# Performance work log

Measured on AMD Instinct MI355X. Metric: run time of the kernel, lower is better.

The kernel has to match this reference:

```python
import jax, jax.numpy as jnp
from jax import lax
import numpy as np

NLAYERS = 3
NHID = 256
NINP = 128
K = 2          # nstride (conv kernel size)
B = 32
W = 512


def _lstm_conv_layer(x_list, hid, ctx, conv_ws, conv_bs, rw, rb, aw):
    """One LSTM_conv(nl=len(conv_ws)) forward.
    x_list: list of [B, H, W]; hid: [nl+1, B, H, K]; ctx: [nl, B, H, K].
    Returns hx_all [B,H,W], cx_all [B,H,W], attn [B,W-1].
    """
    nl = len(conv_ws)
    ig = None
    for j in range(nl):
        # left-pad with last K-1 hidden columns, 'VALID' conv of kernel K -> length W
        padded = jnp.concatenate([hid[j][:, :, 1:], x_list[j]], axis=2)  # [B,H,W+K-1]
        y = lax.conv_general_dilated(padded, conv_ws[j], (1,), 'VALID',
                                     dimension_numbers=('NCH', 'OIH', 'NCH'))
        y = y + conv_bs[j][None, :, None]
        ig = y if ig is None else ig + y          # [B, 4H, W]

    hx0 = hid[nl][:, :, K - 1]                    # [B, H]
    cx0 = ctx[nl - 1][:, :, K - 1]                # [B, H]
    wsz = ig.shape[-1]
    ig_t = jnp.transpose(ig, (2, 0, 1))           # [W, B, 4H]
    not_last = jnp.arange(wsz) < (wsz - 1)

    def step(carry, inp):
        hx, cx = carry
        g_t, nl_flag = inp
        gates = g_t + hx @ rw.T + rb              # [B, 4H]
        i_g, f_g, c_g, o_g = jnp.split(gates, 4, axis=-1)  # torch fused LSTM order
        cx = jax.nn.sigmoid(f_g) * cx + jax.nn.sigmoid(i_g) * jnp.tanh(c_g)
        hx = jax.nn.sigmoid(o_g) * jnp.tanh(cx)
        a = jax.nn.sigmoid(hx @ aw)               # [B]
        hx = jnp.where(nl_flag, hx * a[:, None], hx)  # gate applied except at last step
        return (hx, cx), (hx, cx, a)

    _, (hs, cs, a_s) = lax.scan(step, (hx0, cx0), (ig_t, not_last))
    hx_all = jnp.transpose(hs, (1, 2, 0))         # [B, H, W]
    cx_all = jnp.transpose(cs, (1, 2, 0))
    attn = a_s[:-1].T                             # [B, W-1]
    return hx_all, cx_all, attn


def setup_inputs() -> dict:
    key = jax.random.key(0)
    ks = jax.random.split(key, 10)
    s = 0.02
    return {
        'input':   jax.random.normal(ks[0], (B, NINP, W), jnp.float32),
        'hidden':  jax.random.normal(ks[1], (NLAYERS + 1, B, NHID, K), jnp.float32),
        'context': jax.random.normal(ks[2], (NLAYERS, B, NHID, K), jnp.float32),
        'emb_w':   jax.random.normal(ks[3], (NHID, NINP), jnp.float32) * s,
        'emb_b':   jax.random.normal(ks[4], (NHID,), jnp.float32) * s,
        'conv_w':  jax.random.normal(ks[5], (6, 4 * NHID, NHID, K), jnp.float32) * s,
        'conv_b':  jax.random.normal(ks[6], (6, 4 * NHID), jnp.float32) * s,
        'rec_w':   jax.random.normal(ks[7], (NLAYERS, 4 * NHID, NHID), jnp.float32) * s,
        'rec_b':   jax.random.normal(ks[8], (NLAYERS, 4 * NHID), jnp.float32) * s,
        'attn_w':  jax.random.normal(ks[9], (NLAYERS, NHID), jnp.float32) * s,
    }


def reference(input, hidden, context, emb_w, emb_b, conv_w, conv_b, rec_w, rec_b, attn_w):
    # emb: Conv1d(ninp, nhid, 1)
    x0 = jnp.einsum('oc,bcw->bow', emb_w, input) + emb_b[None, :, None]  # [B,H,W]
    x_list = [x0]
    next_ctx = []
    attns = []
    off = 0
    for l in range(NLAYERS):
        nl = l + 1
        hx_all, cx_all, attn = _lstm_conv_layer(
            x_list, hidden[:nl + 1], context[:nl],
            [conv_w[off + j] for j in range(nl)],
            [conv_b[off + j] for j in range(nl)],
            rec_w[l], rec_b[l], attn_w[l])
        off += nl
        x_list.append(hx_all)
        next_ctx.append(cx_all)
        attns.append(attn)
    x = jnp.stack(x_list, 0)                      # [NLAYERS+1, B, H, W]
    nc = jnp.stack(next_ctx, 0)                   # [NLAYERS, B, H, W]
    attns = jnp.stack(attns, 0)                   # [NLAYERS, B, W-1]
    return x[:, :, :, -K:], nc[:, :, :, -K:], attns
```

## Files before the change

### kernel.cpp

```cpp
#include <hip/hip_runtime.h>


typedef _Float16 h2 __attribute__((ext_vector_type(2)));

static __device__ __forceinline__ float fdot2(unsigned a, unsigned b, float c) {
#if __has_builtin(__builtin_amdgcn_fdot2)
  return __builtin_amdgcn_fdot2(__builtin_bit_cast(h2, a),
                                __builtin_bit_cast(h2, b), c, false);
#else
  h2 x = __builtin_bit_cast(h2, a), y = __builtin_bit_cast(h2, b);
  return c + (float)x[0] * (float)y[0] + (float)x[1] * (float)y[1];
#endif
}

static __device__ __forceinline__ unsigned short f16b(float v) {
  _Float16 h = (_Float16)v;
  return __builtin_bit_cast(unsigned short, h);
}

static __device__ __forceinline__ float sigm(float x) {
  return 1.0f / (1.0f + __expf(-x));
}
static __device__ __forceinline__ float tanh_(float x) {
  return 1.0f - 2.0f / (1.0f + __expf(2.0f * x));
}

__global__ __launch_bounds__(256) void prep_rw(const float* __restrict__ rw,
                                               unsigned* __restrict__ rwp) {
  int idx = blockIdx.x * 256 + threadIdx.x;
  if (idx >= 3 * 131072) return;
  int l = idx / 131072, pos = idx % 131072;
  int tid, rl, j;
  if (pos < 98304) {
    int d = pos >> 9;
    tid = pos & 511;
    rl = d / 24;
    j = d % 24;
  } else {
    int p = pos - 98304;
    int c = p >> 11, rem = p & 2047;
    tid = rem >> 2;
    int k = rem & 3;
    rl = c >> 1;
    j = 24 + (c & 1) * 4 + k;
  }
  int s = tid & 3, u = tid >> 2;
  int row = (rl >> 1) * 256 + (rl & 1) * 128 + u;
  int cp = s * 32 + j;
  const float* src = rw + (l * 1024 + row) * 256 + 2 * cp;
  rwp[idx] = (unsigned)f16b(src[0]) | ((unsigned)f16b(src[1]) << 16);
}

__global__ __launch_bounds__(256) void prep_cw(const float* __restrict__ cw,
                                               unsigned* __restrict__ cwp) {
  int idx = blockIdx.x * 256 + threadIdx.x;
  if (idx >= 6 * 1024 * 2 * 128) return;
  int d = idx & 127, k = (idx >> 7) & 1, o = (idx >> 8) & 1023, jj = idx >> 18;
  const float* src = cw + ((jj * 1024 + o) * 256 + 2 * d) * 2 + k;
  unsigned v = (unsigned)f16b(src[0]) | ((unsigned)f16b(src[2]) << 16);
  cwp[idx] = v;
}

__global__ __launch_bounds__(256) void emb_kernel(
    const float* __restrict__ inp, const float* __restrict__ ew,
    const float* __restrict__ eb, unsigned short* __restrict__ x0f,
    float* __restrict__ out) {
  __shared__ float xt[32][65];
  __shared__ float wt[64][33];
  int b = blockIdx.z, w0 = blockIdx.x * 64, h0 = blockIdx.y * 64;
  int tid = threadIdx.x, tx = tid & 15, ty = tid >> 4;
  float acc[4][4] = {};
  for (int c0 = 0; c0 < 128; c0 += 32) {
    __syncthreads();
#pragma unroll
    for (int i = 0; i < 8; i++) {
      int f = i * 256 + tid, c = f >> 6, wl = f & 63;
      xt[c][wl] = inp[(b * 128 + c0 + c) * 512 + w0 + wl];
    }
#pragma unroll
    for (int i = 0; i < 8; i++) {
      int f = i * 256 + tid, h = f >> 5, c = f & 31;
      wt[h][c] = ew[(h0 + h) * 128 + c0 + c];
    }
    __syncthreads();
#pragma unroll
    for (int c = 0; c < 32; c++) {
      float xv[4], wv[4];
#pragma unroll
      for (int q = 0; q < 4; q++) xv[q] = xt[c][ty * 4 + q];
#pragma unroll
      for (int p = 0; p < 4; p++) wv[p] = wt[tx * 4 + p][c];
#pragma unroll
      for (int q = 0; q < 4; q++)
#pragma unroll
        for (int p = 0; p < 4; p++) acc[q][p] += xv[q] * wv[p];
    }
  }
#pragma unroll
  for (int q = 0; q < 4; q++) {
    int w = w0 + ty * 4 + q;
#pragma unroll
    for (int p = 0; p < 4; p++) {
      int h = h0 + tx * 4 + p;
      float v = acc[q][p] + eb[h];
      x0f[(b * 512 + w) * 256 + h] = f16b(v);
      if (w >= 510) out[(b * 256 + h) * 2 + (w - 510)] = v;
    }
  }
}

__global__ __launch_bounds__(256) void conv_kernel(
    const unsigned short* __restrict__ xf, const unsigned* __restrict__ cwp,
    const float* __restrict__ cb, const float* __restrict__ hidden,
    unsigned short* __restrict__ igf, int l, int off) {
  __shared__ __align__(16) unsigned xs[65][20];
  __shared__ __align__(16) unsigned wsm[2][16][66];
  int b = blockIdx.z, w0 = blockIdx.x * 64, o0 = blockIdx.y * 64;
  int tid = threadIdx.x, tx = tid & 15, ty = tid >> 4;
  float acc[4][4] = {};
  int nl = l + 1;
  for (int j = 0; j < nl; j++) {
    const unsigned* xj = (const unsigned*)(xf + j * 4194304 + b * 512 * 256);
    const unsigned* cwj = cwp + (off + j) * 262144;
    for (int c0 = 0; c0 < 256; c0 += 32) {
      int d0 = c0 >> 1;
      __syncthreads();
#pragma unroll
      for (int i = 0; i < 5; i++) {
        int f = i * 256 + tid;
        if (f < 1040) {
          int col = f >> 4, dw = f & 15;
          int w = w0 - 1 + col;
          unsigned v;
          if (w >= 0) {
            v = xj[w * 128 + d0 + dw];
          } else {
            const float* hp = hidden + ((j * 32 + b) * 256 + 2 * (d0 + dw)) * 2 + 1;
            v = (unsigned)f16b(hp[0]) | ((unsigned)f16b(hp[2]) << 16);
          }
          xs[col][dw] = v;
        }
      }
#pragma unroll
      for (int i = 0; i < 8; i++) {
        int f = i * 256 + tid;
        int oo = f >> 5, k = (f >> 4) & 1, dw = f & 15;
        wsm[k][dw][oo] = cwj[(o0 + oo) * 256 + k * 128 + d0 + dw];
      }
      __syncthreads();
#pragma unroll
      for (int g = 0; g < 4; g++) {
        uint4 xv[5];
#pragma unroll
        for (int q = 0; q < 5; q++)
          xv[q] = *(const uint4*)&xs[ty * 4 + q][g * 4];
#pragma unroll
        for (int p = 0; p < 4; p++) {
          unsigned wv0[4], wv1[4];
#pragma unroll
          for (int r = 0; r < 4; r++) {
            wv0[r] = wsm[0][g * 4 + r][tx * 4 + p];
            wv1[r] = wsm[1][g * 4 + r][tx * 4 + p];
          }
#pragma unroll
          for (int q = 0; q < 4; q++) {
            float a = acc[q][p];
            a = fdot2(wv0[0], xv[q].x, a);
            a = fdot2(wv0[1], xv[q].y, a);
            a = fdot2(wv0[2], xv[q].z, a);
            a = fdot2(wv0[3], xv[q].w, a);
            a = fdot2(wv1[0], xv[q + 1].x, a);
            a = fdot2(wv1[1], xv[q + 1].y, a);
            a = fdot2(wv1[2], xv[q + 1].z, a);
            a = fdot2(wv1[3], xv[q + 1].w, a);
            acc[q][p] = a;
          }
        }
      }
    }
  }
#pragma unroll
  for (int p = 0; p < 4; p++) {
    int o = o0 + tx * 4 + p;
    float bias = 0.f;
    for (int j = 0; j < nl; j++) bias += cb[(off + j) * 1024 + o];
#pragma unroll
    for (int q = 0; q < 4; q++) {
      int w = w0 + ty * 4 + q;
      igf[(b * 512 + w) * 1024 + o] = f16b(acc[q][p] + bias);
    }
  }
}

__global__ __launch_bounds__(512)
__attribute__((amdgpu_waves_per_eu(2, 2)))
void rec_kernel(const _Float16* __restrict__ igf, const unsigned* __restrict__ rwp_l,
                const float* __restrict__ rb, const float* __restrict__ aw,
                const float* __restrict__ hidden, const float* __restrict__ context,
                int l, unsigned short* __restrict__ xnext, float* __restrict__ out) {
  __shared__ __align__(16) uint4 w_lds4[16 * 512];
  __shared__ __align__(16) unsigned short hx_buf[2][256];
  __shared__ float red[2][8];
  int b = blockIdx.x, tid = threadIdx.x;
  int s = tid & 3, u = tid >> 2, lane = tid & 63, wid = tid >> 6;
  int hh = s & 1;
  int u2 = u + 128 * hh;

  unsigned wv[192];
#pragma unroll
  for (int d = 0; d < 192; d++) wv[d] = rwp_l[d * 512 + tid];
#pragma unroll
  for (int d = 0; d < 192; d++) asm volatile("" : "+v"(wv[d]));

  {
    const uint4* g16 = (const uint4*)(rwp_l + 98304);
#pragma unroll
    for (int c = 0; c < 16; c++) w_lds4[c * 512 + tid] = g16[c * 512 + tid];
  }

  float rb0 = rb[u2], rb1 = rb[256 + u2], rb2 = rb[512 + u2], rb3 = rb[768 + u2];
  float awj = aw[u2];
  float cx = context[((l * 32 + b) * 256 + u2) * 2 + 1];
  if (tid < 256)
    hx_buf[1][tid] = f16b(hidden[(((l + 1) * 32 + b) * 256 + tid) * 2 + 1]);
  float h_prev = 0.f;
  __syncthreads();

  const _Float16* igb = igf + (b * 512) * 1024 + u2;

  for (int t = 0; t < 512; t++) {
    int cur = t & 1, prv = cur ^ 1;
    const _Float16* ip = igb + t * 1024;
    float ig0 = (float)ip[0], ig1 = (float)ip[256];
    float ig2 = (float)ip[512], ig3 = (float)ip[768];
    float m_ = 1.0f;
    if (t) {
      const float* rp = red[prv];
      m_ = sigm(((rp[0] + rp[1]) + (rp[2] + rp[3])) +
                ((rp[4] + rp[5]) + (rp[6] + rp[7])));
    }

    float acc[8] = {};
    const uint4* hq = ((const uint4*)hx_buf[prv]) + 8 * s;
#pragma unroll
    for (int q = 0; q < 6; q++) {
      uint4 h = hq[q];
#pragma unroll
      for (int rl = 0; rl < 8; rl++) {
        acc[rl] = fdot2(wv[rl * 24 + q * 4 + 0], h.x, acc[rl]);
        acc[rl] = fdot2(wv[rl * 24 + q * 4 + 1], h.y, acc[rl]);
        acc[rl] = fdot2(wv[rl * 24 + q * 4 + 2], h.z, acc[rl]);
        acc[rl] = fdot2(wv[rl * 24 + q * 4 + 3], h.w, acc[rl]);
      }
    }
#pragma unroll
    for (int q = 6; q < 8; q++) {
      uint4 h = hq[q];
#pragma unroll
      for (int rl = 0; rl < 8; rl++) {
        uint4 lw = w_lds4[(rl * 2 + (q - 6)) * 512 + tid];
        acc[rl] = fdot2(lw.x, h.x, acc[rl]);
        acc[rl] = fdot2(lw.y, h.y, acc[rl]);
        acc[rl] = fdot2(lw.z, h.z, acc[rl]);
        acc[rl] = fdot2(lw.w, h.w, acc[rl]);
      }
    }
#pragma unroll
    for (int rl = 0; rl < 8; rl++) acc[rl] += __shfl_xor(acc[rl], 1);
#pragma unroll
    for (int rl = 0; rl < 8; rl++) acc[rl] += __shfl_xor(acc[rl], 2);

    float di = hh ? acc[1] : acc[0];
    float df = hh ? acc[3] : acc[2];
    float dc = hh ? acc[5] : acc[4];
    float do_ = hh ? acc[7] : acc[6];
    float g_i = ig0 + rb0 + m_ * di;
    float g_f = ig1 + rb1 + m_ * df;
    float g_c = ig2 + rb2 + m_ * dc;
    float g_o = ig3 + rb3 + m_ * do_;
    cx = sigm(g_f) * cx + sigm(g_i) * tanh_(g_c);
    float h_raw = sigm(g_o) * tanh_(cx);

    float part = (s < 2) ? h_raw * awj : 0.f;
#pragma unroll
    for (int sh = 32; sh > 0; sh >>= 1) part += __shfl_xor(part, sh);
    if (lane == 0) red[cur][wid] = part;

    if (s < 2) {
      hx_buf[cur][u2] = f16b(h_raw);
      if (t) {
        float hg = h_prev * m_;
        xnext[(b * 512 + (t - 1)) * 256 + u2] = f16b(hg);
        if (t == 511)
          out[(((l + 1) * 32 + b) * 256 + u2) * 2 + 0] = hg;
      }
      if (t >= 510)
        out[65536 + ((l * 32 + b) * 256 + u2) * 2 + (t - 510)] = cx;
    }
    if (tid == 0 && t) out[114688 + (l * 32 + b) * 511 + (t - 1)] = m_;
    h_prev = h_raw;
    __syncthreads();
  }
  if (s < 2) {
    xnext[(b * 512 + 511) * 256 + u2] = f16b(h_prev);
    out[(((l + 1) * 32 + b) * 256 + u2) * 2 + 1] = h_prev;
  }
}

extern "C" void kernel_launch(void* const* d_in, const int* in_sizes, int n_in,
                              void* d_out, int out_size, void* d_ws,
                              size_t ws_size, hipStream_t stream) {
  const float* input  = (const float*)d_in[0];
  const float* hidden = (const float*)d_in[1];
  const float* context= (const float*)d_in[2];
  const float* emb_w  = (const float*)d_in[3];
  const float* emb_b  = (const float*)d_in[4];
  const float* conv_w = (const float*)d_in[5];
  const float* conv_b = (const float*)d_in[6];
  const float* rec_w  = (const float*)d_in[7];
  const float* rec_b  = (const float*)d_in[8];
  const float* attn_w = (const float*)d_in[9];
  float* out = (float*)d_out;

  char* ws = (char*)d_ws;
  unsigned short* xf16 = (unsigned short*)ws;
  _Float16* igf = (_Float16*)(ws + 33554432);
  unsigned* rwp = (unsigned*)(ws + 67108864);
  unsigned* cwp = (unsigned*)(ws + 68681728);

  hipLaunchKernelGGL(prep_rw, dim3(1536), dim3(256), 0, stream, rec_w, rwp);
  hipLaunchKernelGGL(prep_cw, dim3(6144), dim3(256), 0, stream, conv_w, cwp);
  hipLaunchKernelGGL(emb_kernel, dim3(8, 4, 32), dim3(256), 0, stream,
                     input, emb_w, emb_b, xf16, out);
  int off = 0;
  for (int l = 0; l < 3; l++) {
    hipLaunchKernelGGL(conv_kernel, dim3(8, 16, 32), dim3(256), 0, stream,
                       xf16, cwp, conv_b, hidden, (unsigned short*)igf, l, off);
    hipLaunchKernelGGL(rec_kernel, dim3(32), dim3(512), 0, stream,
                       igf, rwp + l * 131072, rec_b + l * 1024,
                       attn_w + l * 256, hidden, context, l,
                       xf16 + (l + 1) * 4194304, out);
    off += l + 1;
  }
}
```

Measured before the change: 4.405 ms.

## Store recurrent weights in AGPRs, stream a slice from global, use DPP reductions

Recurrent weights are moved from arch VGPRs into accumulation registers (AGPRs) via inline v_accvgpr writes and reads. One column slice of the weights is now streamed from global memory each step instead of being kept in registers. The h-vector read offsets are rotated per lane group to avoid LDS bank conflicts, and the shuffle-based reductions are replaced by DPP row operations. Global output stores are moved to the start of the next step so they leave the critical path. This relieves VGPR pressure at the cost of extra AGPR read instructions and per-step global loads.

New measurement: 6.175 ms. 40.2% more time.

```diff
diff --git a/kernel.cpp b/kernel.cpp
--- a/kernel.cpp
+++ b/kernel.cpp
@@ -13,6 +13,19 @@
 #endif
 }
 
+static __device__ __forceinline__ unsigned aread(unsigned a) {
+  unsigned v;
+  asm volatile("v_accvgpr_read_b32 %0, %1" : "=v"(v) : "a"(a));
+  return v;
+}
+
+template <int CTRL>
+static __device__ __forceinline__ float dpp_add(float x) {
+  int t = __builtin_amdgcn_update_dpp(0, __builtin_bit_cast(int, x), CTRL, 0xf,
+                                      0xf, true);
+  return x + __builtin_bit_cast(float, t);
+}
+
 static __device__ __forceinline__ unsigned short f16b(float v) {
   _Float16 h = (_Float16)v;
   return __builtin_bit_cast(unsigned short, h);
@@ -30,23 +43,39 @@
   int idx = blockIdx.x * 256 + threadIdx.x;
   if (idx >= 3 * 131072) return;
   int l = idx / 131072, pos = idx % 131072;
-  int tid, rl, j;
-  if (pos < 98304) {
+  int tid, rl, i, k;
+  if (pos < 90112) {
     int d = pos >> 9;
     tid = pos & 511;
-    rl = d / 24;
-    j = d % 24;
+    if (d < 160) {
+      rl = d / 20;
+      int rem = d % 20;
+      i = rem >> 2;
+      k = rem & 3;
+    } else {
+      rl = 4 + ((d - 160) >> 2);
+      i = 5;
+      k = (d - 160) & 3;
+    }
+  } else if (pos < 98304) {
+    int p = pos - 90112;
+    rl = p >> 11;
+    int rem = p & 2047;
+    tid = rem >> 2;
+    k = rem & 3;
+    i = 5;
   } else {
     int p = pos - 98304;
     int c = p >> 11, rem = p & 2047;
     tid = rem >> 2;
-    int k = rem & 3;
+    k = rem & 3;
     rl = c >> 1;
-    j = 24 + (c & 1) * 4 + k;
+    i = 6 + (c & 1);
   }
   int s = tid & 3, u = tid >> 2;
   int row = (rl >> 1) * 256 + (rl & 1) * 128 + u;
-  int cp = s * 32 + j;
+  int qeff = (i + 2 * s) & 7;
+  int cp = s * 32 + qeff * 4 + k;
   const float* src = rw + (l * 1024 + row) * 256 + 2 * cp;
   rwp[idx] = (unsigned)f16b(src[0]) | ((unsigned)f16b(src[1]) << 16);
 }
@@ -206,17 +235,23 @@
   int hh = s & 1;
   int u2 = u + 128 * hh;
 
-  unsigned wv[192];
-#pragma unroll
-  for (int d = 0; d < 192; d++) wv[d] = rwp_l[d * 512 + tid];
-#pragma unroll
-  for (int d = 0; d < 192; d++) asm volatile("" : "+v"(wv[d]));
+  unsigned wa[176];
+#pragma unroll
+  for (int d = 0; d < 176; d++) {
+    unsigned v = rwp_l[d * 512 + tid];
+    asm volatile("v_accvgpr_write_b32 %0, %1" : "=a"(wa[d]) : "v"(v));
+  }
 
   {
     const uint4* g16 = (const uint4*)(rwp_l + 98304);
 #pragma unroll
     for (int c = 0; c < 16; c++) w_lds4[c * 512 + tid] = g16[c * 512 + tid];
   }
+  const uint4* gq = ((const uint4*)rwp_l) + 22528;
+
+  int qoff[8];
+#pragma unroll
+  for (int i = 0; i < 8; i++) qoff[i] = (8 * s + ((i + 2 * s) & 7)) * 16;
 
   float rb0 = rb[u2], rb1 = rb[256 + u2], rb2 = rb[512 + u2], rb3 = rb[768 + u2];
   float awj = aw[u2];
@@ -230,35 +265,72 @@
 
   for (int t = 0; t < 512; t++) {
     int cur = t & 1, prv = cur ^ 1;
-    const _Float16* ip = igb + t * 1024;
-    float ig0 = (float)ip[0], ig1 = (float)ip[256];
-    float ig2 = (float)ip[512], ig3 = (float)ip[768];
     float m_ = 1.0f;
     if (t) {
       const float* rp = red[prv];
       m_ = sigm(((rp[0] + rp[1]) + (rp[2] + rp[3])) +
                 ((rp[4] + rp[5]) + (rp[6] + rp[7])));
-    }
+      if (s < 2) {
+        float hg = h_prev * m_;
+        xnext[(b * 512 + (t - 1)) * 256 + u2] = f16b(hg);
+        if (t == 511) {
+          out[(((l + 1) * 32 + b) * 256 + u2) * 2 + 0] = hg;
+          out[65536 + ((l * 32 + b) * 256 + u2) * 2 + 0] = cx;
+        }
+      }
+      if (tid == 0) out[114688 + (l * 32 + b) * 511 + (t - 1)] = m_;
+    }
+    const _Float16* ip = igb + t * 1024;
+    float ig0 = (float)ip[0], ig1 = (float)ip[256];
+    float ig2 = (float)ip[512], ig3 = (float)ip[768];
+    uint4 gw0 = gq[tid], gw1 = gq[512 + tid], gw2 = gq[1024 + tid],
+          gw3 = gq[1536 + tid];
 
     float acc[8] = {};
-    const uint4* hq = ((const uint4*)hx_buf[prv]) + 8 * s;
-#pragma unroll
-    for (int q = 0; q < 6; q++) {
-      uint4 h = hq[q];
+    const char* hb = (const char*)hx_buf[prv];
+#pragma unroll
+    for (int i = 0; i < 5; i++) {
+      uint4 h = *(const uint4*)(hb + qoff[i]);
 #pragma unroll
       for (int rl = 0; rl < 8; rl++) {
-        acc[rl] = fdot2(wv[rl * 24 + q * 4 + 0], h.x, acc[rl]);
-        acc[rl] = fdot2(wv[rl * 24 + q * 4 + 1], h.y, acc[rl]);
-        acc[rl] = fdot2(wv[rl * 24 + q * 4 + 2], h.z, acc[rl]);
-        acc[rl] = fdot2(wv[rl * 24 + q * 4 + 3], h.w, acc[rl]);
-      }
-    }
-#pragma unroll
-    for (int q = 6; q < 8; q++) {
-      uint4 h = hq[q];
+        acc[rl] = fdot2(aread(wa[rl * 20 + i * 4 + 0]), h.x, acc[rl]);
+        acc[rl] = fdot2(aread(wa[rl * 20 + i * 4 + 1]), h.y, acc[rl]);
+        acc[rl] = fdot2(aread(wa[rl * 20 + i * 4 + 2]), h.z, acc[rl]);
+        acc[rl] = fdot2(aread(wa[rl * 20 + i * 4 + 3]), h.w, acc[rl]);
+      }
+    }
+    {
+      uint4 h = *(const uint4*)(hb + qoff[5]);
+      acc[0] = fdot2(gw0.x, h.x, acc[0]);
+      acc[0] = fdot2(gw0.y, h.y, acc[0]);
+      acc[0] = fdot2(gw0.z, h.z, acc[0]);
+      acc[0] = fdot2(gw0.w, h.w, acc[0]);
+      acc[1] = fdot2(gw1.x, h.x, acc[1]);
+      acc[1] = fdot2(gw1.y, h.y, acc[1]);
+      acc[1] = fdot2(gw1.z, h.z, acc[1]);
+      acc[1] = fdot2(gw1.w, h.w, acc[1]);
+      acc[2] = fdot2(gw2.x, h.x, acc[2]);
+      acc[2] = fdot2(gw2.y, h.y, acc[2]);
+      acc[2] = fdot2(gw2.z, h.z, acc[2]);
+      acc[2] = fdot2(gw2.w, h.w, acc[2]);
+      acc[3] = fdot2(gw3.x, h.x, acc[3]);
+      acc[3] = fdot2(gw3.y, h.y, acc[3]);
+      acc[3] = fdot2(gw3.z, h.z, acc[3]);
+      acc[3] = fdot2(gw3.w, h.w, acc[3]);
+#pragma unroll
+      for (int rl = 4; rl < 8; rl++) {
+        acc[rl] = fdot2(aread(wa[160 + (rl - 4) * 4 + 0]), h.x, acc[rl]);
+        acc[rl] = fdot2(aread(wa[160 + (rl - 4) * 4 + 1]), h.y, acc[rl]);
+        acc[rl] = fdot2(aread(wa[160 + (rl - 4) * 4 + 2]), h.z, acc[rl]);
+        acc[rl] = fdot2(aread(wa[160 + (rl - 4) * 4 + 3]), h.w, acc[rl]);
+      }
+    }
+#pragma unroll
+    for (int i = 6; i < 8; i++) {
+      uint4 h = *(const uint4*)(hb + qoff[i]);
 #pragma unroll
       for (int rl = 0; rl < 8; rl++) {
-        uint4 lw = w_lds4[(rl * 2 + (q - 6)) * 512 + tid];
+        uint4 lw = w_lds4[(rl * 2 + (i - 6)) * 512 + tid];
         acc[rl] = fdot2(lw.x, h.x, acc[rl]);
         acc[rl] = fdot2(lw.y, h.y, acc[rl]);
         acc[rl] = fdot2(lw.z, h.z, acc[rl]);
@@ -266,9 +338,9 @@
       }
     }
 #pragma unroll
-    for (int rl = 0; rl < 8; rl++) acc[rl] += __shfl_xor(acc[rl], 1);
-#pragma unroll
-    for (int rl = 0; rl < 8; rl++) acc[rl] += __shfl_xor(acc[rl], 2);
+    for (int rl = 0; rl < 8; rl++) acc[rl] = dpp_add<0xB1>(acc[rl]);
+#pragma unroll
+    for (int rl = 0; rl < 8; rl++) acc[rl] = dpp_add<0x4E>(acc[rl]);
 
     float di = hh ? acc[1] : acc[0];
     float df = hh ? acc[3] : acc[2];
@@ -281,29 +353,24 @@
     cx = sigm(g_f) * cx + sigm(g_i) * tanh_(g_c);
     float h_raw = sigm(g_o) * tanh_(cx);
 
+    if (s < 2) hx_buf[cur][u2] = f16b(h_raw);
+
     float part = (s < 2) ? h_raw * awj : 0.f;
-#pragma unroll
-    for (int sh = 32; sh > 0; sh >>= 1) part += __shfl_xor(part, sh);
-    if (lane == 0) red[cur][wid] = part;
-
-    if (s < 2) {
-      hx_buf[cur][u2] = f16b(h_raw);
-      if (t) {
-        float hg = h_prev * m_;
-        xnext[(b * 512 + (t - 1)) * 256 + u2] = f16b(hg);
-        if (t == 511)
-          out[(((l + 1) * 32 + b) * 256 + u2) * 2 + 0] = hg;
-      }
-      if (t >= 510)
-        out[65536 + ((l * 32 + b) * 256 + u2) * 2 + (t - 510)] = cx;
-    }
-    if (tid == 0 && t) out[114688 + (l * 32 + b) * 511 + (t - 1)] = m_;
+    part = dpp_add<0x111>(part);
+    part = dpp_add<0x112>(part);
+    part = dpp_add<0x114>(part);
+    part = dpp_add<0x118>(part);
+    part = dpp_add<0x142>(part);
+    part = dpp_add<0x143>(part);
+    if (lane == 63) red[cur][wid] = part;
+
     h_prev = h_raw;
     __syncthreads();
   }
   if (s < 2) {
     xnext[(b * 512 + 511) * 256 + u2] = f16b(h_prev);
     out[(((l + 1) * 32 + b) * 256 + u2) * 2 + 1] = h_prev;
+    out[65536 + ((l * 32 + b) * 256 + u2) * 2 + 1] = cx;
   }
 }
 
```
